# Kernel optimization log

Measured on AMD Instinct MI355X. Metric: run time of the kernel, lower is better.

## Reference

```python
import jax, jax.numpy as jnp
import numpy as np
from math import sqrt

HEADS = 16
DIM_HEAD = 64
EPS = 1e-4
MP_T = 0.3


def l2norm(t, eps=EPS):
    n = jnp.linalg.norm(t, axis=-1, keepdims=True)
    return t / jnp.maximum(n, eps)


def mp_linear(x, w):
    # weight-normalized linear: l2norm rows / sqrt(fan_in)
    fan_in = w.shape[1]
    wn = l2norm(w) / sqrt(fan_in)
    return x @ wn.T


def setup_inputs() -> dict:
    key = jax.random.key(0)
    k1, k2, k3, k4 = jax.random.split(key, 4)
    b, n, dim = 2, 2048, 1024
    x = jax.random.normal(k1, (b, n, dim), dtype=jnp.float32)
    w_qkv = jax.random.normal(k2, (3 * HEADS * DIM_HEAD, dim), dtype=jnp.float32)
    w_out = jax.random.normal(k3, (dim, HEADS * DIM_HEAD), dtype=jnp.float32)
    mem_kv = jax.random.normal(k4, (2, HEADS, 4, DIM_HEAD), dtype=jnp.float32)
    return {"x": x, "w_qkv": w_qkv, "w_out": w_out, "mem_kv": mem_kv}


def reference(x, w_qkv, w_out, mem_kv):
    b, n, dim = x.shape
    h, d = HEADS, DIM_HEAD
    scale = d ** -0.5

    qkv = mp_linear(x, w_qkv)                      # [b, n, 3*h*d]
    q, k, v = jnp.split(qkv, 3, axis=-1)
    split_heads = lambda t: t.reshape(b, n, h, d).transpose(0, 2, 1, 3)  # b h n d
    q, k, v = map(split_heads, (q, k, v))

    mk = jnp.broadcast_to(mem_kv[0], (b, h, mem_kv.shape[2], d))
    mv = jnp.broadcast_to(mem_kv[1], (b, h, mem_kv.shape[2], d))
    k = jnp.concatenate([mk, k], axis=2)
    v = jnp.concatenate([mv, v], axis=2)

    # pixel_norm: l2 normalize over head dim, rescale by sqrt(d)
    pn = lambda t: l2norm(t) * sqrt(d)
    q, k, v = pn(q), pn(k), pn(v)

    q = q * scale
    sim = jnp.einsum('bhid,bhjd->bhij', q, k)
    attn = jax.nn.softmax(sim, axis=-1)
    out = jnp.einsum('bhij,bhjd->bhid', attn, v)
    out = out.transpose(0, 2, 1, 3).reshape(b, n, h * d)
    out = mp_linear(out, w_out)

    # magnitude-preserving residual add
    t = MP_T
    return (out * (1.0 - t) + x * t) / sqrt((1.0 - t) ** 2 + t ** 2)
```

## Files before the change

kernel.cpp:

```cpp
#include <hip/hip_runtime.h>
#include <hip/hip_bf16.h>
#include <math.h>


#define EPSN 1e-4f
#define LDH 72
#define NKEY 2112
#define LOG2E 1.4426950408889634f

typedef __attribute__((ext_vector_type(8))) short short8;
typedef __attribute__((ext_vector_type(4))) short short4v;
typedef __attribute__((ext_vector_type(4))) float floatx4;

typedef __attribute__((address_space(1))) const void g_void;
typedef __attribute__((address_space(3))) void lds_void;

__device__ __forceinline__ void async16(void* lds, const void* g) {
    __builtin_amdgcn_global_load_lds((g_void*)g, (lds_void*)lds, 16, 0, 0);
}

__device__ __forceinline__ short f2bf(float f) {
    union { float f; unsigned u; } c{f};
    unsigned r = (c.u + 0x7FFF + ((c.u >> 16) & 1)) >> 16;
    return (short)r;
}
__device__ __forceinline__ short f2bf_fast(float f) {
    union { float f; unsigned u; } c{f};
    return (short)((c.u + 0x8000) >> 16);
}
__device__ __forceinline__ float bf2f(short s) {
    union { unsigned u; float f; } c;
    c.u = ((unsigned)(unsigned short)s) << 16;
    return c.f;
}

__global__ __launch_bounds__(256) void cast_bf16(const float* __restrict__ in,
                                                 short* __restrict__ out) {
    int i = (blockIdx.x * 256 + threadIdx.x) * 4;
    float4 v = *(const float4*)(in + i);
    short4v s = {f2bf(v.x), f2bf(v.y), f2bf(v.z), f2bf(v.w)};
    *(short4v*)(out + i) = s;
}

__global__ __launch_bounds__(256) void norm_rows(const float* __restrict__ w,
                                                 short* __restrict__ wn, int cols) {
    __shared__ float red[256];
    int r = blockIdx.x;
    const float* row = w + (size_t)r * cols;
    float ss = 0.0f;
    for (int c = threadIdx.x; c < cols; c += 256) { float v = row[c]; ss += v * v; }
    red[threadIdx.x] = ss;
    __syncthreads();
    for (int s = 128; s > 0; s >>= 1) {
        if (threadIdx.x < s) red[threadIdx.x] += red[threadIdx.x + s];
        __syncthreads();
    }
    float f = 1.0f / (fmaxf(sqrtf(red[0]), EPSN) * 32.0f);
    for (int c = threadIdx.x; c < cols; c += 256) wn[(size_t)r * cols + c] = f2bf(row[c] * f);
}

template<int MT, int NT>
__global__ __launch_bounds__(256) void gemm_mfma(const short* __restrict__ A,
                                                 const short* __restrict__ B,
                                                 float* __restrict__ C,
                                                 short* __restrict__ Cb,
                                                 int M, int N, int K,
                                                 const float* __restrict__ resid) {
    constexpr int FI = MT / 32;
    constexpr int FJ = NT / 32;
    constexpr int nA = MT / 64;
    constexpr int nB = NT / 64;
    __shared__ __align__(16) short As[2][MT * 32];
    __shared__ __align__(16) short Bs[2][NT * 32];
    const int tid = threadIdx.x;
    const int wv = tid >> 6, lane = tid & 63;
    const int l16 = lane & 15, quad = lane >> 4;
    const int wr = wv >> 1, wc = wv & 1;
    const int bm0 = blockIdx.y * MT, bn0 = blockIdx.x * NT;
    const int grow = lane >> 2;
    const int gk = (lane & 3) * 8;

    floatx4 acc[FI][FJ];
    #pragma unroll
    for (int i = 0; i < FI; i++)
        #pragma unroll
        for (int j = 0; j < FJ; j++) acc[i][j] = (floatx4){0.f, 0.f, 0.f, 0.f};

    const short* Abase = A + (size_t)(bm0 + wv * (MT / 4) + grow) * K + gk;
    const short* Bbase = B + (size_t)(bn0 + wv * (NT / 4) + grow) * K + gk;

    #pragma unroll
    for (int j = 0; j < nA; j++)
        async16(&As[0][(wv * (MT / 4) + j * 16) * 32], Abase + (size_t)(j * 16) * K);
    #pragma unroll
    for (int j = 0; j < nB; j++)
        async16(&Bs[0][(wv * (NT / 4) + j * 16) * 32], Bbase + (size_t)(j * 16) * K);

    const int NKI = K >> 5;
    for (int ki = 0; ki < NKI; ki++) {
        const int cur = ki & 1;
        if (ki + 1 < NKI) {
            const int nxt = cur ^ 1;
            const int off = (ki + 1) * 32;
            #pragma unroll
            for (int j = 0; j < nA; j++)
                async16(&As[nxt][(wv * (MT / 4) + j * 16) * 32], Abase + (size_t)(j * 16) * K + off);
            #pragma unroll
            for (int j = 0; j < nB; j++)
                async16(&Bs[nxt][(wv * (NT / 4) + j * 16) * 32], Bbase + (size_t)(j * 16) * K + off);
            if constexpr (nA + nB == 4)
                asm volatile("s_waitcnt vmcnt(4)" ::: "memory");
            else
                asm volatile("s_waitcnt vmcnt(2)" ::: "memory");
        } else {
            asm volatile("s_waitcnt vmcnt(0)" ::: "memory");
        }
        asm volatile("s_barrier" ::: "memory");
        short8 aA[FI], bB[FJ];
        #pragma unroll
        for (int i = 0; i < FI; i++)
            aA[i] = *(const short8*)&As[cur][(wr * (MT / 2) + i * 16 + l16) * 32 + quad * 8];
        #pragma unroll
        for (int j = 0; j < FJ; j++)
            bB[j] = *(const short8*)&Bs[cur][(wc * (NT / 2) + j * 16 + l16) * 32 + quad * 8];
        #pragma unroll
        for (int i = 0; i < FI; i++)
            #pragma unroll
            for (int j = 0; j < FJ; j++)
                acc[i][j] = __builtin_amdgcn_mfma_f32_16x16x32_bf16(aA[i], bB[j], acc[i][j], 0, 0, 0);
        asm volatile("s_barrier" ::: "memory");
    }
    #pragma unroll
    for (int i = 0; i < FI; i++)
        #pragma unroll
        for (int j = 0; j < FJ; j++)
            #pragma unroll
            for (int r = 0; r < 4; r++) {
                const int row = bm0 + wr * (MT / 2) + i * 16 + quad * 4 + r;
                const int col = bn0 + wc * (NT / 2) + j * 16 + l16;
                const size_t idx = (size_t)row * N + col;
                float v = acc[i][j][r];
                if (resid) v = (v * 0.7f + resid[idx] * 0.3f) * 1.3130643285972254f;
                if (Cb) Cb[idx] = f2bf(v);
                else    C[idx]  = v;
            }
}

__global__ __launch_bounds__(256) void prep_qkv(const short* __restrict__ qkvb,
                                                const float* __restrict__ memkv,
                                                short* __restrict__ Qb,
                                                short* __restrict__ Kb,
                                                short* __restrict__ Vt) {
    __shared__ short Ls[64 * LDH];
    const int bh = blockIdx.x, bb = bh >> 4, h = bh & 15;
    const int tile = blockIdx.y;
    const int tid = threadIdx.x;
    const int r = tid >> 2, part = tid & 3;

    if (tile < 32) {
        const int tok = tile * 64 + r;
        const short* base = qkvb + ((size_t)(bb * 2048 + tok)) * 3072 + h * 64 + part * 16;
        float q[16], k[16], v[16];
        float ssq = 0.f, ssk = 0.f, ssv = 0.f;
        short8 a0 = *(const short8*)base,          a1 = *(const short8*)(base + 8);
        short8 b0 = *(const short8*)(base + 1024), b1 = *(const short8*)(base + 1032);
        short8 c0 = *(const short8*)(base + 2048), c1 = *(const short8*)(base + 2056);
        #pragma unroll
        for (int i = 0; i < 8; i++) {
            q[i] = bf2f(a0[i]); q[8+i] = bf2f(a1[i]);
            k[i] = bf2f(b0[i]); k[8+i] = bf2f(b1[i]);
            v[i] = bf2f(c0[i]); v[8+i] = bf2f(c1[i]);
        }
        #pragma unroll
        for (int i = 0; i < 16; i++) { ssq += q[i]*q[i]; ssk += k[i]*k[i]; ssv += v[i]*v[i]; }
        ssq += __shfl_xor(ssq, 1); ssq += __shfl_xor(ssq, 2);
        ssk += __shfl_xor(ssk, 1); ssk += __shfl_xor(ssk, 2);
        ssv += __shfl_xor(ssv, 1); ssv += __shfl_xor(ssv, 2);
        const float fq = LOG2E / fmaxf(sqrtf(ssq), EPSN);
        const float fk = 8.0f / fmaxf(sqrtf(ssk), EPSN);
        const float fv = 8.0f / fmaxf(sqrtf(ssv), EPSN);
        short8 oq, ok, oq1, ok1;
        #pragma unroll
        for (int i = 0; i < 8; i++) { oq[i] = f2bf(q[i] * fq); ok[i] = f2bf(k[i] * fk); }
        #pragma unroll
        for (int i = 0; i < 8; i++) { oq1[i] = f2bf(q[8+i] * fq); ok1[i] = f2bf(k[8+i] * fk); }
        short* qd = Qb + ((size_t)bh * 2048 + tok) * 64 + part * 16;
        *(short8*)qd = oq; *(short8*)(qd + 8) = oq1;
        short* kd = Kb + ((size_t)bh * NKEY + 4 + tok) * 64 + part * 16;
        *(short8*)kd = ok; *(short8*)(kd + 8) = ok1;
        #pragma unroll
        for (int i = 0; i < 16; i++) Ls[r * LDH + part * 16 + i] = f2bf(v[i] * fv);
        __syncthreads();
        short4v o[4];
        #pragma unroll
        for (int j = 0; j < 16; j++) o[j >> 2][j & 3] = Ls[(part * 16 + j) * LDH + r];
        short* vd = Vt + ((size_t)bh * 64 + r) * NKEY + 4 + tile * 64 + part * 16;
        #pragma unroll
        for (int j = 0; j < 4; j++) *(short4v*)(vd + j * 4) = o[j];
    } else {
        if (r < 4) {
            const float* pk = memkv + (size_t)(h * 4 + r) * 64 + part * 16;
            const float* pv = memkv + (size_t)((16 + h) * 4 + r) * 64 + part * 16;
            float k[16], v[16]; float ssk = 0.f, ssv = 0.f;
            #pragma unroll
            for (int i = 0; i < 16; i += 4) {
                float4 a = *(const float4*)(pk + i);
                float4 b = *(const float4*)(pv + i);
                k[i]=a.x; k[i+1]=a.y; k[i+2]=a.z; k[i+3]=a.w;
                v[i]=b.x; v[i+1]=b.y; v[i+2]=b.z; v[i+3]=b.w;
                ssk += a.x*a.x + a.y*a.y + a.z*a.z + a.w*a.w;
                ssv += b.x*b.x + b.y*b.y + b.z*b.z + b.w*b.w;
            }
            ssk += __shfl_xor(ssk, 1); ssk += __shfl_xor(ssk, 2);
            ssv += __shfl_xor(ssv, 1); ssv += __shfl_xor(ssv, 2);
            const float fk = 8.0f / fmaxf(sqrtf(ssk), EPSN);
            const float fv = 8.0f / fmaxf(sqrtf(ssv), EPSN);
            short* kd = Kb + ((size_t)bh * NKEY + r) * 64 + part * 16;
            #pragma unroll
            for (int i = 0; i < 16; i++) kd[i] = f2bf(k[i] * fk);
            #pragma unroll
            for (int i = 0; i < 16; i++)
                Vt[((size_t)bh * 64 + part * 16 + i) * NKEY + r] = f2bf(v[i] * fv);
        }
        for (int p = tid; p < 480; p += 256)
            *(short8*)(Kb + ((size_t)bh * NKEY + 2052) * 64 + p * 8) = (short8){0,0,0,0,0,0,0,0};
        for (int p = tid; p < 960; p += 256) {
            int row = p / 15, c = p % 15;
            *(short4v*)(Vt + ((size_t)bh * 64 + row) * NKEY + 2052 + c * 4) = (short4v){0,0,0,0};
        }
    }
}

__global__ __launch_bounds__(512) void attn_mfma(const short* __restrict__ Qb,
                                                 const short* __restrict__ Kb,
                                                 const short* __restrict__ Vt,
                                                 short* __restrict__ out) {
    const int bh = blockIdx.x;
    const int q0 = blockIdx.y * 128;
    const int tid = threadIdx.x;
    const int wave = tid >> 6;
    const int lane = tid & 63;
    const int l16 = lane & 15;
    const int quad = lane >> 4;

    __shared__ __align__(16) short Ks[64 * LDH];
    __shared__ __align__(16) short Vs[64 * LDH];
    __shared__ __align__(16) short Ps[8][16 * LDH];

    const short* qp = Qb + ((size_t)bh * 2048 + q0 + wave * 16 + l16) * 64 + quad * 8;
    short8 aQ0 = *(const short8*)qp;
    short8 aQ1 = *(const short8*)(qp + 32);

    floatx4 O[4];
    #pragma unroll
    for (int t = 0; t < 4; t++) O[t] = (floatx4){0.f, 0.f, 0.f, 0.f};
    float lp[4] = {0.f, 0.f, 0.f, 0.f};

    const int srow = tid >> 3, sch = tid & 7;
    for (int tile = 0; tile < 33; tile++) {
        __syncthreads();
        {
            short8 kv = *(const short8*)(Kb + ((size_t)bh * NKEY + tile * 64 + srow) * 64 + sch * 8);
            *(short8*)&Ks[srow * LDH + sch * 8] = kv;
            short8 vv = *(const short8*)(Vt + ((size_t)bh * 64 + srow) * NKEY + tile * 64 + sch * 8);
            *(short8*)&Vs[srow * LDH + sch * 8] = vv;
        }
        __syncthreads();

        floatx4 S[4];
        #pragma unroll
        for (int t = 0; t < 4; t++) {
            const short* pb = &Ks[(t * 16 + l16) * LDH + quad * 8];
            short8 b0 = *(const short8*)pb;
            short8 b1 = *(const short8*)(pb + 32);
            floatx4 s = (floatx4){-12.f, -12.f, -12.f, -12.f};
            s = __builtin_amdgcn_mfma_f32_16x16x32_bf16(aQ0, b0, s, 0, 0, 0);
            s = __builtin_amdgcn_mfma_f32_16x16x32_bf16(aQ1, b1, s, 0, 0, 0);
            S[t] = s;
        }
        if (tile == 32) {
            #pragma unroll
            for (int t = 0; t < 4; t++)
                if (t * 16 + l16 >= 4) { S[t][0] = S[t][1] = S[t][2] = S[t][3] = -1e30f; }
        }
        short* pp = Ps[wave];
        #pragma unroll
        for (int t = 0; t < 4; t++) {
            #pragma unroll
            for (int i = 0; i < 4; i++) {
                float p = __builtin_amdgcn_exp2f(S[t][i]);
                lp[i] += p;
                pp[(quad * 4 + i) * LDH + t * 16 + l16] = f2bf_fast(p);
            }
        }
        short8 aP0, aP1;
        {
            const short* pa = &pp[l16 * LDH + quad * 8];
            aP0 = *(const short8*)pa;
            aP1 = *(const short8*)(pa + 32);
        }
        #pragma unroll
        for (int t = 0; t < 4; t++) {
            const short* pv2 = &Vs[(t * 16 + l16) * LDH + quad * 8];
            short8 b0 = *(const short8*)pv2;
            short8 b1 = *(const short8*)(pv2 + 32);
            O[t] = __builtin_amdgcn_mfma_f32_16x16x32_bf16(aP0, b0, O[t], 0, 0, 0);
            O[t] = __builtin_amdgcn_mfma_f32_16x16x32_bf16(aP1, b1, O[t], 0, 0, 0);
        }
    }

    const int bb = bh >> 4, h = bh & 15;
    #pragma unroll
    for (int i = 0; i < 4; i++) {
        float s = lp[i];
        s += __shfl_xor(s, 1); s += __shfl_xor(s, 2);
        s += __shfl_xor(s, 4); s += __shfl_xor(s, 8);
        const float inv = 1.0f / s;
        const int qrow = q0 + wave * 16 + quad * 4 + i;
        const size_t base = ((size_t)(bb * 2048 + qrow)) * 1024 + h * 64 + l16;
        #pragma unroll
        for (int t = 0; t < 4; t++) out[base + t * 16] = f2bf(O[t][i] * inv);
    }
}

extern "C" void kernel_launch(void* const* d_in, const int* in_sizes, int n_in,
                              void* d_out, int out_size, void* d_ws, size_t ws_size,
                              hipStream_t stream) {
    const float* x      = (const float*)d_in[0];
    const float* w_qkv  = (const float*)d_in[1];
    const float* w_out  = (const float*)d_in[2];
    const float* mem_kv = (const float*)d_in[3];
    float* out = (float*)d_out;

    char* ws = (char*)d_ws;
    short* wnqkv_b = (short*)(ws);
    short* wnout_b = (short*)(ws + (6u << 20));
    short* xb      = (short*)(ws + (8u << 20));
    short* qkvb    = (short*)(ws + (16u << 20));
    short* attnb   = (short*)(ws + (40u << 20));
    short* Qb      = (short*)(ws + (48u << 20));
    short* Kb      = (short*)(ws + (56u << 20));
    short* Vt      = (short*)(ws + (65u << 20));

    cast_bf16<<<4096, 256, 0, stream>>>(x, xb);
    norm_rows<<<3072, 256, 0, stream>>>(w_qkv, wnqkv_b, 1024);
    norm_rows<<<1024, 256, 0, stream>>>(w_out, wnout_b, 1024);

    gemm_mfma<128, 128><<<dim3(3072 / 128, 4096 / 128), 256, 0, stream>>>(
        xb, wnqkv_b, nullptr, qkvb, 4096, 3072, 1024, nullptr);

    prep_qkv<<<dim3(32, 33), 256, 0, stream>>>(qkvb, mem_kv, Qb, Kb, Vt);

    attn_mfma<<<dim3(32, 16), 512, 0, stream>>>(Qb, Kb, Vt, attnb);

    gemm_mfma<64, 64><<<dim3(1024 / 64, 4096 / 64), 256, 0, stream>>>(
        attnb, wnout_b, out, nullptr, 4096, 1024, 1024, x);
}
```

Before: 230.5 us.

## Fuse QKV pixel-norm into GEMM epilogue, merge prep kernels, double-buffer attention

Merges the input cast, both weight row-normalisations and the memory-KV setup into one prep launch. The QKV GEMM epilogue now computes each head's L2 norm in registers and writes scaled Q, K and transposed V directly, which removes the intermediate qkv buffer and the separate prep_qkv pass. Attention now stages K/V tiles with async global-to-LDS loads into a double buffer so loads overlap compute. The output GEMM switches to 128x64 tiles. The risk is that the fused epilogue writes V with strided stores and uses more registers.

```diff
diff --git a/kernel.cpp b/kernel.cpp
--- a/kernel.cpp
+++ b/kernel.cpp
@@ -28,42 +28,189 @@
     union { float f; unsigned u; } c{f};
     return (short)((c.u + 0x8000) >> 16);
 }
-__device__ __forceinline__ float bf2f(short s) {
-    union { unsigned u; float f; } c;
-    c.u = ((unsigned)(unsigned short)s) << 16;
-    return c.f;
-}
-
-__global__ __launch_bounds__(256) void cast_bf16(const float* __restrict__ in,
-                                                 short* __restrict__ out) {
-    int i = (blockIdx.x * 256 + threadIdx.x) * 4;
-    float4 v = *(const float4*)(in + i);
-    short4v s = {f2bf(v.x), f2bf(v.y), f2bf(v.z), f2bf(v.w)};
-    *(short4v*)(out + i) = s;
-}
-
-__global__ __launch_bounds__(256) void norm_rows(const float* __restrict__ w,
-                                                 short* __restrict__ wn, int cols) {
-    __shared__ float red[256];
-    int r = blockIdx.x;
-    const float* row = w + (size_t)r * cols;
-    float ss = 0.0f;
-    for (int c = threadIdx.x; c < cols; c += 256) { float v = row[c]; ss += v * v; }
-    red[threadIdx.x] = ss;
-    __syncthreads();
-    for (int s = 128; s > 0; s >>= 1) {
-        if (threadIdx.x < s) red[threadIdx.x] += red[threadIdx.x + s];
+
+__global__ __launch_bounds__(256) void prep_inputs(const float* __restrict__ x,
+                                                   const float* __restrict__ w_qkv,
+                                                   const float* __restrict__ w_out,
+                                                   const float* __restrict__ memkv,
+                                                   short* __restrict__ xb,
+                                                   short* __restrict__ wnqkv,
+                                                   short* __restrict__ wnout,
+                                                   short* __restrict__ Kb,
+                                                   short* __restrict__ Vt) {
+    const int bid = blockIdx.x, tid = threadIdx.x;
+    if (bid < 4096) {
+        int i = bid * 1024 + tid * 4;
+        float4 v = *(const float4*)(x + i);
+        short4v s = {f2bf(v.x), f2bf(v.y), f2bf(v.z), f2bf(v.w)};
+        *(short4v*)(xb + i) = s;
+        return;
+    }
+    if (bid < 8192) {
+        const float* w; short* wn; int r;
+        if (bid < 7168) { w = w_qkv; wn = wnqkv; r = bid - 4096; }
+        else            { w = w_out; wn = wnout; r = bid - 7168; }
+        __shared__ float red[256];
+        const float* row = w + (size_t)r * 1024;
+        float ss = 0.f;
+        for (int c = tid; c < 1024; c += 256) { float v = row[c]; ss += v * v; }
+        red[tid] = ss;
         __syncthreads();
-    }
-    float f = 1.0f / (fmaxf(sqrtf(red[0]), EPSN) * 32.0f);
-    for (int c = threadIdx.x; c < cols; c += 256) wn[(size_t)r * cols + c] = f2bf(row[c] * f);
+        for (int s = 128; s > 0; s >>= 1) {
+            if (tid < s) red[tid] += red[tid + s];
+            __syncthreads();
+        }
+        float f = 1.0f / (fmaxf(sqrtf(red[0]), EPSN) * 32.0f);
+        for (int c = tid; c < 1024; c += 256) wn[(size_t)r * 1024 + c] = f2bf(row[c] * f);
+        return;
+    }
+    const int bh = bid - 8192, h = bh & 15;
+    const int r = tid >> 2, part = tid & 3;
+    if (r < 4) {
+        const float* pk = memkv + (size_t)(h * 4 + r) * 64 + part * 16;
+        const float* pv = memkv + (size_t)((16 + h) * 4 + r) * 64 + part * 16;
+        float k[16], v[16]; float ssk = 0.f, ssv = 0.f;
+        #pragma unroll
+        for (int i = 0; i < 16; i += 4) {
+            float4 a = *(const float4*)(pk + i);
+            float4 b = *(const float4*)(pv + i);
+            k[i]=a.x; k[i+1]=a.y; k[i+2]=a.z; k[i+3]=a.w;
+            v[i]=b.x; v[i+1]=b.y; v[i+2]=b.z; v[i+3]=b.w;
+            ssk += a.x*a.x + a.y*a.y + a.z*a.z + a.w*a.w;
+            ssv += b.x*b.x + b.y*b.y + b.z*b.z + b.w*b.w;
+        }
+        ssk += __shfl_xor(ssk, 1); ssk += __shfl_xor(ssk, 2);
+        ssv += __shfl_xor(ssv, 1); ssv += __shfl_xor(ssv, 2);
+        const float fk = 8.0f / fmaxf(sqrtf(ssk), EPSN);
+        const float fv = 8.0f / fmaxf(sqrtf(ssv), EPSN);
+        short* kd = Kb + ((size_t)bh * NKEY + r) * 64 + part * 16;
+        #pragma unroll
+        for (int i = 0; i < 16; i++) kd[i] = f2bf(k[i] * fk);
+        #pragma unroll
+        for (int i = 0; i < 16; i++)
+            Vt[((size_t)bh * 64 + part * 16 + i) * NKEY + r] = f2bf(v[i] * fv);
+    }
+    for (int p = tid; p < 480; p += 256)
+        *(short8*)(Kb + ((size_t)bh * NKEY + 2052) * 64 + p * 8) = (short8){0,0,0,0,0,0,0,0};
+    for (int p = tid; p < 960; p += 256) {
+        int row = p / 15, c = p % 15;
+        *(short4v*)(Vt + ((size_t)bh * 64 + row) * NKEY + 2052 + c * 4) = (short4v){0,0,0,0};
+    }
+}
+
+__global__ __launch_bounds__(256) void gemm_qkv(const short* __restrict__ A,
+                                                const short* __restrict__ B,
+                                                short* __restrict__ Qb,
+                                                short* __restrict__ Kb,
+                                                short* __restrict__ Vt) {
+    constexpr int K = 1024;
+    __shared__ __align__(16) short As[2][128 * 32];
+    __shared__ __align__(16) short Bs[2][128 * 32];
+    const int tid = threadIdx.x;
+    const int wv = tid >> 6, lane = tid & 63;
+    const int l16 = lane & 15, quad = lane >> 4;
+    const int wr = wv >> 1, wc = wv & 1;
+    const int bm0 = blockIdx.y * 128, bn0 = blockIdx.x * 128;
+    const int grow = lane >> 2;
+    const int gk = (lane & 3) * 8;
+
+    floatx4 acc[4][4];
+    #pragma unroll
+    for (int i = 0; i < 4; i++)
+        #pragma unroll
+        for (int j = 0; j < 4; j++) acc[i][j] = (floatx4){0.f, 0.f, 0.f, 0.f};
+
+    const short* Abase = A + (size_t)(bm0 + wv * 32 + grow) * K + gk;
+    const short* Bbase = B + (size_t)(bn0 + wv * 32 + grow) * K + gk;
+
+    #pragma unroll
+    for (int j = 0; j < 2; j++) {
+        async16(&As[0][(wv * 32 + j * 16) * 32], Abase + (size_t)(j * 16) * K);
+        async16(&Bs[0][(wv * 32 + j * 16) * 32], Bbase + (size_t)(j * 16) * K);
+    }
+    const int NKI = K >> 5;
+    for (int ki = 0; ki < NKI; ki++) {
+        const int cur = ki & 1;
+        if (ki + 1 < NKI) {
+            const int nxt = cur ^ 1;
+            const int off = (ki + 1) * 32;
+            #pragma unroll
+            for (int j = 0; j < 2; j++) {
+                async16(&As[nxt][(wv * 32 + j * 16) * 32], Abase + (size_t)(j * 16) * K + off);
+                async16(&Bs[nxt][(wv * 32 + j * 16) * 32], Bbase + (size_t)(j * 16) * K + off);
+            }
+            asm volatile("s_waitcnt vmcnt(4)" ::: "memory");
+        } else {
+            asm volatile("s_waitcnt vmcnt(0)" ::: "memory");
+        }
+        asm volatile("s_barrier" ::: "memory");
+        short8 aA[4], bB[4];
+        #pragma unroll
+        for (int i = 0; i < 4; i++)
+            aA[i] = *(const short8*)&As[cur][(wr * 64 + i * 16 + l16) * 32 + quad * 8];
+        #pragma unroll
+        for (int j = 0; j < 4; j++)
+            bB[j] = *(const short8*)&Bs[cur][(wc * 64 + j * 16 + l16) * 32 + quad * 8];
+        #pragma unroll
+        for (int i = 0; i < 4; i++)
+            #pragma unroll
+            for (int j = 0; j < 4; j++)
+                acc[i][j] = __builtin_amdgcn_mfma_f32_16x16x32_bf16(aA[i], bB[j], acc[i][j], 0, 0, 0);
+        asm volatile("s_barrier" ::: "memory");
+    }
+
+    const int colbase = bn0 + wc * 64;
+    const int which = colbase >> 10;
+    const int h = (colbase >> 6) & 15;
+    float sc[4][4];
+    #pragma unroll
+    for (int i = 0; i < 4; i++)
+        #pragma unroll
+        for (int r = 0; r < 4; r++) {
+            float ss = 0.f;
+            #pragma unroll
+            for (int j = 0; j < 4; j++) ss += acc[i][j][r] * acc[i][j][r];
+            ss += __shfl_xor(ss, 1); ss += __shfl_xor(ss, 2);
+            ss += __shfl_xor(ss, 4); ss += __shfl_xor(ss, 8);
+            const float num = (which == 0) ? LOG2E : 8.0f;
+            sc[i][r] = num / fmaxf(sqrtf(ss), EPSN);
+        }
+    if (which == 2) {
+        #pragma unroll
+        for (int i = 0; i < 4; i++) {
+            const int row0 = bm0 + wr * 64 + i * 16 + quad * 4;
+            const int bh = (row0 >> 11) * 16 + h;
+            const int tok0 = row0 & 2047;
+            #pragma unroll
+            for (int j = 0; j < 4; j++) {
+                const int d = j * 16 + l16;
+                short4v o = {f2bf(acc[i][j][0] * sc[i][0]), f2bf(acc[i][j][1] * sc[i][1]),
+                             f2bf(acc[i][j][2] * sc[i][2]), f2bf(acc[i][j][3] * sc[i][3])};
+                *(short4v*)(Vt + ((size_t)bh * 64 + d) * NKEY + 4 + tok0) = o;
+            }
+        }
+    } else {
+        #pragma unroll
+        for (int i = 0; i < 4; i++)
+            #pragma unroll
+            for (int r = 0; r < 4; r++) {
+                const int row = bm0 + wr * 64 + i * 16 + quad * 4 + r;
+                const int bh = (row >> 11) * 16 + h;
+                const int tok = row & 2047;
+                const size_t base = (which == 0) ? ((size_t)bh * 2048 + tok) * 64
+                                                 : ((size_t)bh * NKEY + 4 + tok) * 64;
+                short* dst = (which == 0) ? Qb : Kb;
+                #pragma unroll
+                for (int j = 0; j < 4; j++)
+                    dst[base + j * 16 + l16] = f2bf(acc[i][j][r] * sc[i][r]);
+            }
+    }
 }
 
 template<int MT, int NT>
 __global__ __launch_bounds__(256) void gemm_mfma(const short* __restrict__ A,
                                                  const short* __restrict__ B,
                                                  float* __restrict__ C,
-                                                 short* __restrict__ Cb,
                                                  int M, int N, int K,
                                                  const float* __restrict__ resid) {
     constexpr int FI = MT / 32;
@@ -108,10 +255,9 @@
             #pragma unroll
             for (int j = 0; j < nB; j++)
                 async16(&Bs[nxt][(wv * (NT / 4) + j * 16) * 32], Bbase + (size_t)(j * 16) * K + off);
-            if constexpr (nA + nB == 4)
-                asm volatile("s_waitcnt vmcnt(4)" ::: "memory");
-            else
-                asm volatile("s_waitcnt vmcnt(2)" ::: "memory");
+            if constexpr (nA + nB == 4)      asm volatile("s_waitcnt vmcnt(4)" ::: "memory");
+            else if constexpr (nA + nB == 3) asm volatile("s_waitcnt vmcnt(3)" ::: "memory");
+            else                             asm volatile("s_waitcnt vmcnt(2)" ::: "memory");
         } else {
             asm volatile("s_waitcnt vmcnt(0)" ::: "memory");
         }
@@ -141,94 +287,8 @@
                 const size_t idx = (size_t)row * N + col;
                 float v = acc[i][j][r];
                 if (resid) v = (v * 0.7f + resid[idx] * 0.3f) * 1.3130643285972254f;
-                if (Cb) Cb[idx] = f2bf(v);
-                else    C[idx]  = v;
+                C[idx] = v;
             }
-}
-
-__global__ __launch_bounds__(256) void prep_qkv(const short* __restrict__ qkvb,
-                                                const float* __restrict__ memkv,
-                                                short* __restrict__ Qb,
-                                                short* __restrict__ Kb,
-                                                short* __restrict__ Vt) {
-    __shared__ short Ls[64 * LDH];
-    const int bh = blockIdx.x, bb = bh >> 4, h = bh & 15;
-    const int tile = blockIdx.y;
-    const int tid = threadIdx.x;
-    const int r = tid >> 2, part = tid & 3;
-
-    if (tile < 32) {
-        const int tok = tile * 64 + r;
-        const short* base = qkvb + ((size_t)(bb * 2048 + tok)) * 3072 + h * 64 + part * 16;
-        float q[16], k[16], v[16];
-        float ssq = 0.f, ssk = 0.f, ssv = 0.f;
-        short8 a0 = *(const short8*)base,          a1 = *(const short8*)(base + 8);
-        short8 b0 = *(const short8*)(base + 1024), b1 = *(const short8*)(base + 1032);
-        short8 c0 = *(const short8*)(base + 2048), c1 = *(const short8*)(base + 2056);
-        #pragma unroll
-        for (int i = 0; i < 8; i++) {
-            q[i] = bf2f(a0[i]); q[8+i] = bf2f(a1[i]);
-            k[i] = bf2f(b0[i]); k[8+i] = bf2f(b1[i]);
-            v[i] = bf2f(c0[i]); v[8+i] = bf2f(c1[i]);
-        }
-        #pragma unroll
-        for (int i = 0; i < 16; i++) { ssq += q[i]*q[i]; ssk += k[i]*k[i]; ssv += v[i]*v[i]; }
-        ssq += __shfl_xor(ssq, 1); ssq += __shfl_xor(ssq, 2);
-        ssk += __shfl_xor(ssk, 1); ssk += __shfl_xor(ssk, 2);
-        ssv += __shfl_xor(ssv, 1); ssv += __shfl_xor(ssv, 2);
-        const float fq = LOG2E / fmaxf(sqrtf(ssq), EPSN);
-        const float fk = 8.0f / fmaxf(sqrtf(ssk), EPSN);
-        const float fv = 8.0f / fmaxf(sqrtf(ssv), EPSN);
-        short8 oq, ok, oq1, ok1;
-        #pragma unroll
-        for (int i = 0; i < 8; i++) { oq[i] = f2bf(q[i] * fq); ok[i] = f2bf(k[i] * fk); }
-        #pragma unroll
-        for (int i = 0; i < 8; i++) { oq1[i] = f2bf(q[8+i] * fq); ok1[i] = f2bf(k[8+i] * fk); }
-        short* qd = Qb + ((size_t)bh * 2048 + tok) * 64 + part * 16;
-        *(short8*)qd = oq; *(short8*)(qd + 8) = oq1;
-        short* kd = Kb + ((size_t)bh * NKEY + 4 + tok) * 64 + part * 16;
-        *(short8*)kd = ok; *(short8*)(kd + 8) = ok1;
-        #pragma unroll
-        for (int i = 0; i < 16; i++) Ls[r * LDH + part * 16 + i] = f2bf(v[i] * fv);
-        __syncthreads();
-        short4v o[4];
-        #pragma unroll
-        for (int j = 0; j < 16; j++) o[j >> 2][j & 3] = Ls[(part * 16 + j) * LDH + r];
-        short* vd = Vt + ((size_t)bh * 64 + r) * NKEY + 4 + tile * 64 + part * 16;
-        #pragma unroll
-        for (int j = 0; j < 4; j++) *(short4v*)(vd + j * 4) = o[j];
-    } else {
-        if (r < 4) {
-            const float* pk = memkv + (size_t)(h * 4 + r) * 64 + part * 16;
-            const float* pv = memkv + (size_t)((16 + h) * 4 + r) * 64 + part * 16;
-            float k[16], v[16]; float ssk = 0.f, ssv = 0.f;
-            #pragma unroll
-            for (int i = 0; i < 16; i += 4) {
-                float4 a = *(const float4*)(pk + i);
-                float4 b = *(const float4*)(pv + i);
-                k[i]=a.x; k[i+1]=a.y; k[i+2]=a.z; k[i+3]=a.w;
-                v[i]=b.x; v[i+1]=b.y; v[i+2]=b.z; v[i+3]=b.w;
-                ssk += a.x*a.x + a.y*a.y + a.z*a.z + a.w*a.w;
-                ssv += b.x*b.x + b.y*b.y + b.z*b.z + b.w*b.w;
-            }
-            ssk += __shfl_xor(ssk, 1); ssk += __shfl_xor(ssk, 2);
-            ssv += __shfl_xor(ssv, 1); ssv += __shfl_xor(ssv, 2);
-            const float fk = 8.0f / fmaxf(sqrtf(ssk), EPSN);
-            const float fv = 8.0f / fmaxf(sqrtf(ssv), EPSN);
-            short* kd = Kb + ((size_t)bh * NKEY + r) * 64 + part * 16;
-            #pragma unroll
-            for (int i = 0; i < 16; i++) kd[i] = f2bf(k[i] * fk);
-            #pragma unroll
-            for (int i = 0; i < 16; i++)
-                Vt[((size_t)bh * 64 + part * 16 + i) * NKEY + r] = f2bf(v[i] * fv);
-        }
-        for (int p = tid; p < 480; p += 256)
-            *(short8*)(Kb + ((size_t)bh * NKEY + 2052) * 64 + p * 8) = (short8){0,0,0,0,0,0,0,0};
-        for (int p = tid; p < 960; p += 256) {
-            int row = p / 15, c = p % 15;
-            *(short4v*)(Vt + ((size_t)bh * 64 + row) * NKEY + 2052 + c * 4) = (short4v){0,0,0,0};
-        }
-    }
 }
 
 __global__ __launch_bounds__(512) void attn_mfma(const short* __restrict__ Qb,
@@ -238,41 +298,58 @@
     const int bh = blockIdx.x;
     const int q0 = blockIdx.y * 128;
     const int tid = threadIdx.x;
-    const int wave = tid >> 6;
-    const int lane = tid & 63;
-    const int l16 = lane & 15;
-    const int quad = lane >> 4;
-
-    __shared__ __align__(16) short Ks[64 * LDH];
-    __shared__ __align__(16) short Vs[64 * LDH];
+    const int wave = tid >> 6, lane = tid & 63;
+    const int l16 = lane & 15, quad = lane >> 4;
+
+    __shared__ __align__(16) short Ks2[2][2][64 * 32];
+    __shared__ __align__(16) short Vs2[2][2][64 * 32];
     __shared__ __align__(16) short Ps[8][16 * LDH];
 
     const short* qp = Qb + ((size_t)bh * 2048 + q0 + wave * 16 + l16) * 64 + quad * 8;
     short8 aQ0 = *(const short8*)qp;
     short8 aQ1 = *(const short8*)(qp + 32);
+    asm volatile("s_waitcnt vmcnt(0)" ::: "memory");
+
+    const int grow = lane >> 2, gsub = (lane & 3) * 8;
+    const int u0 = wave * 2;
+    auto issue = [&](int tile, int buf) {
+        #pragma unroll
+        for (int s = 0; s < 2; s++) {
+            const int u = u0 + s;
+            const int hh = (u >> 2) & 1;
+            const int L = u & 3;
+            const int rr = L * 16 + grow;
+            const int cc = hh * 32 + gsub;
+            if (u < 8)
+                async16(&Ks2[buf][hh][L * 512],
+                        Kb + ((size_t)bh * NKEY + tile * 64 + rr) * 64 + cc);
+            else
+                async16(&Vs2[buf][hh][L * 512],
+                        Vt + ((size_t)bh * 64 + rr) * NKEY + tile * 64 + cc);
+        }
+    };
 
     floatx4 O[4];
     #pragma unroll
     for (int t = 0; t < 4; t++) O[t] = (floatx4){0.f, 0.f, 0.f, 0.f};
     float lp[4] = {0.f, 0.f, 0.f, 0.f};
 
-    const int srow = tid >> 3, sch = tid & 7;
+    issue(0, 0);
     for (int tile = 0; tile < 33; tile++) {
-        __syncthreads();
-        {
-            short8 kv = *(const short8*)(Kb + ((size_t)bh * NKEY + tile * 64 + srow) * 64 + sch * 8);
-            *(short8*)&Ks[srow * LDH + sch * 8] = kv;
-            short8 vv = *(const short8*)(Vt + ((size_t)bh * 64 + srow) * NKEY + tile * 64 + sch * 8);
-            *(short8*)&Vs[srow * LDH + sch * 8] = vv;
-        }
-        __syncthreads();
+        const int cur = tile & 1;
+        if (tile < 32) {
+            issue(tile + 1, cur ^ 1);
+            asm volatile("s_waitcnt vmcnt(2)" ::: "memory");
+        } else {
+            asm volatile("s_waitcnt vmcnt(0)" ::: "memory");
+        }
+        asm volatile("s_barrier" ::: "memory");
 
         floatx4 S[4];
         #pragma unroll
         for (int t = 0; t < 4; t++) {
-            const short* pb = &Ks[(t * 16 + l16) * LDH + quad * 8];
-            short8 b0 = *(const short8*)pb;
-            short8 b1 = *(const short8*)(pb + 32);
+            short8 b0 = *(const short8*)&Ks2[cur][0][(t * 16 + l16) * 32 + quad * 8];
+            short8 b1 = *(const short8*)&Ks2[cur][1][(t * 16 + l16) * 32 + quad * 8];
             floatx4 s = (floatx4){-12.f, -12.f, -12.f, -12.f};
             s = __builtin_amdgcn_mfma_f32_16x16x32_bf16(aQ0, b0, s, 0, 0, 0);
             s = __builtin_amdgcn_mfma_f32_16x16x32_bf16(aQ1, b1, s, 0, 0, 0);
@@ -301,12 +378,12 @@
         }
         #pragma unroll
         for (int t = 0; t < 4; t++) {
-            const short* pv2 = &Vs[(t * 16 + l16) * LDH + quad * 8];
-            short8 b0 = *(const short8*)pv2;
-            short8 b1 = *(const short8*)(pv2 + 32);
+            short8 b0 = *(const short8*)&Vs2[cur][0][(t * 16 + l16) * 32 + quad * 8];
+            short8 b1 = *(const short8*)&Vs2[cur][1][(t * 16 + l16) * 32 + quad * 8];
             O[t] = __builtin_amdgcn_mfma_f32_16x16x32_bf16(aP0, b0, O[t], 0, 0, 0);
             O[t] = __builtin_amdgcn_mfma_f32_16x16x32_bf16(aP1, b1, O[t], 0, 0, 0);
         }
+        asm volatile("s_barrier" ::: "memory");
     }
 
     const int bb = bh >> 4, h = bh & 15;
@@ -336,23 +413,19 @@
     short* wnqkv_b = (short*)(ws);
     short* wnout_b = (short*)(ws + (6u << 20));
     short* xb      = (short*)(ws + (8u << 20));
-    short* qkvb    = (short*)(ws + (16u << 20));
-    short* attnb   = (short*)(ws + (40u << 20));
-    short* Qb      = (short*)(ws + (48u << 20));
-    short* Kb      = (short*)(ws + (56u << 20));
-    short* Vt      = (short*)(ws + (65u << 20));
-
-    cast_bf16<<<4096, 256, 0, stream>>>(x, xb);
-    norm_rows<<<3072, 256, 0, stream>>>(w_qkv, wnqkv_b, 1024);
-    norm_rows<<<1024, 256, 0, stream>>>(w_out, wnout_b, 1024);
-
-    gemm_mfma<128, 128><<<dim3(3072 / 128, 4096 / 128), 256, 0, stream>>>(
-        xb, wnqkv_b, nullptr, qkvb, 4096, 3072, 1024, nullptr);
-
-    prep_qkv<<<dim3(32, 33), 256, 0, stream>>>(qkvb, mem_kv, Qb, Kb, Vt);
+    short* Qb      = (short*)(ws + (16u << 20));
+    short* Kb      = (short*)(ws + (24u << 20));
+    short* Vt      = (short*)(ws + (33u << 20));
+    short* attnb   = (short*)(ws + (42u << 20));
+
+    prep_inputs<<<8224, 256, 0, stream>>>(x, w_qkv, w_out, mem_kv,
+                                          xb, wnqkv_b, wnout_b, Kb, Vt);
+
+    gemm_qkv<<<dim3(3072 / 128, 4096 / 128), 256, 0, stream>>>(
+        xb, wnqkv_b, Qb, Kb, Vt);
 
     attn_mfma<<<dim3(32, 16), 512, 0, stream>>>(Qb, Kb, Vt, attnb);
 
-    gemm_mfma<64, 64><<<dim3(1024 / 64, 4096 / 64), 256, 0, stream>>>(
-        attnb, wnout_b, out, nullptr, 4096, 1024, 1024, x);
-}
+    gemm_mfma<128, 64><<<dim3(1024 / 64, 4096 / 128), 256, 0, stream>>>(
+        attnb, wnout_b, out, 4096, 1024, 1024, x);
+}
```

Measured after the change: 215.9 us. 6.3% less time.
